# Optimization experiments

Measured on AMD Instinct MI355X. Metric: run time of the kernel, lower is better.

## Reference

```python
import jax, jax.numpy as jnp
import numpy as np

B, T, C, H = 4, 2048, 1024, 16
D = C // H  # head dim = 64


def setup_inputs() -> dict:
    key = jax.random.key(0)
    ks = jax.random.split(key, 5)
    s = 1.0 / np.sqrt(C)
    return {
        "x": jax.random.normal(ks[0], (B, T, C), dtype=jnp.float32),
        "Wq": jax.random.normal(ks[1], (C, C), dtype=jnp.float32) * s,
        "bq": jnp.zeros((C,), dtype=jnp.float32),
        "Wk": jax.random.normal(ks[2], (C, C), dtype=jnp.float32) * s,
        "bk": jnp.zeros((C,), dtype=jnp.float32),
        "Wv": jax.random.normal(ks[3], (C, C), dtype=jnp.float32) * s,
        "bv": jnp.zeros((C,), dtype=jnp.float32),
        "Wp": jax.random.normal(ks[4], (C, C), dtype=jnp.float32) * s,
        "bp": jnp.zeros((C,), dtype=jnp.float32),
    }


def reference(x, Wq, bq, Wk, bk, Wv, bv, Wp, bp):
    Bb, Tt, Cc = x.shape
    # QKV projections (torch Linear: y = x @ W.T + b)
    q = (x @ Wq.T + bq).reshape(Bb, Tt, H, D).transpose(0, 2, 1, 3)  # [B,H,T,D]
    k = (x @ Wk.T + bk).reshape(Bb, Tt, H, D).transpose(0, 2, 1, 3)
    v = (x @ Wv.T + bv).reshape(Bb, Tt, H, D).transpose(0, 2, 1, 3)
    att = jnp.einsum("bhqd,bhkd->bhqk", q, k) / jnp.sqrt(jnp.float32(D))
    causal = jnp.tril(jnp.ones((Tt, Tt), dtype=bool))
    att = jnp.where(causal[None, None], att, -jnp.inf)
    att = jax.nn.softmax(att, axis=-1)
    y = jnp.einsum("bhqk,bhkd->bhqd", att, v)  # [B,H,T,D]
    y = y.transpose(0, 2, 1, 3).reshape(Bb, Tt, Cc)
    return y @ Wp.T + bp
```

## Files before the change

kernel.cpp:

```cpp
#include <hip/hip_runtime.h>

typedef unsigned short u16;
typedef unsigned int u32;

typedef __attribute__((ext_vector_type(4))) float f32x4;
typedef __attribute__((ext_vector_type(8))) short bf16x8;


__device__ inline u16 f2b(float f) {
  union { float f; u32 u; } x; x.f = f;
  u32 u = x.u;
  u32 r = (u + 0x7fffu + ((u >> 16) & 1u)) >> 16;
  return (u16)r;
}

__device__ inline u32 cvtpk(float lo, float hi) {
  u32 r;
  asm("v_cvt_pk_bf16_f32 %0, %1, %2" : "=v"(r) : "v"(lo), "v"(hi));
  return r;
}

__device__ inline void gload_lds16(const void* g, void* l) {
  __builtin_amdgcn_global_load_lds(
      (const __attribute__((address_space(1))) u32*)g,
      (__attribute__((address_space(3))) u32*)l, 16, 0, 0);
}


__global__ __launch_bounds__(256) void cvt_all(const float* __restrict__ x,
                                               const float* __restrict__ w0,
                                               const float* __restrict__ w1,
                                               const float* __restrict__ w2,
                                               const float* __restrict__ w3,
                                               u16* __restrict__ xo,
                                               u16* __restrict__ wo) {
  int b = blockIdx.x;
  const float* s;
  u16* d;
  int i;
  if (b < 8192) {
    s = x; d = xo; i = b * 256 + threadIdx.x;
  } else {
    int m = (b - 8192) >> 10;
    s = (m == 0) ? w0 : (m == 1) ? w1 : (m == 2) ? w2 : w3;
    d = wo + (size_t)m * 1048576;
    i = ((b - 8192) & 1023) * 256 + threadIdx.x;
  }
  float4 v = ((const float4*)s)[i];
  ushort4 o;
  o.x = f2b(v.x); o.y = f2b(v.y); o.z = f2b(v.z); o.w = f2b(v.w);
  ((ushort4*)d)[i] = o;
}


__global__ __launch_bounds__(256) void gemm_qkv(const u16* __restrict__ A,
                                                const u16* __restrict__ W,
                                                const float* __restrict__ bq,
                                                const float* __restrict__ bk,
                                                const float* __restrict__ bv,
                                                u16* __restrict__ outQ,
                                                u16* __restrict__ outK,
                                                u16* __restrict__ outVt,
                                                float qscale) {
  __shared__ u16 sA[8192];
  __shared__ u16 sB[8192];

  const int K = 1024;
  const int t = threadIdx.x;
  const int lane = t & 63;
  const int w = t >> 6;
  const int wr = w >> 1, wc = w & 1;
  const int lr = lane & 15, lg = lane >> 4;

  int bid = blockIdx.y * 24 + blockIdx.x;
  int swz = (bid & 7) * 192 + (bid >> 3);
  const int mBase = (swz / 24) * 128;
  const int nBase = (swz % 24) * 128;
  const int mode = nBase >> 10;

  f32x4 zero = {0.f, 0.f, 0.f, 0.f};
  f32x4 acc[4][4];
#pragma unroll
  for (int i = 0; i < 4; ++i)
#pragma unroll
    for (int j = 0; j < 4; ++j) acc[i][j] = zero;

  const int rA = t >> 2;
  const int cA = (t & 3) * 8;

  for (int k0 = 0; k0 < K; k0 += 64) {
#pragma unroll
    for (int hh = 0; hh < 2; ++hh)
#pragma unroll
      for (int i = 0; i < 2; ++i) {
        gload_lds16(A + (size_t)(mBase + i * 64 + rA) * K + k0 + hh * 32 + cA,
                    &sA[hh * 4096 + i * 2048 + t * 8]);
        gload_lds16(W + (size_t)(nBase + i * 64 + rA) * K + k0 + hh * 32 + cA,
                    &sB[hh * 4096 + i * 2048 + t * 8]);
      }
    __syncthreads();

#pragma unroll
    for (int hh = 0; hh < 2; ++hh) {
      bf16x8 af[4], bf[4];
#pragma unroll
      for (int i = 0; i < 4; ++i)
        af[i] = *(const bf16x8*)&sA[hh * 4096 +
                                    (wr * 64 + i * 16 + lr) * 32 + lg * 8];
#pragma unroll
      for (int j = 0; j < 4; ++j)
        bf[j] = *(const bf16x8*)&sB[hh * 4096 +
                                    (wc * 64 + j * 16 + lr) * 32 + lg * 8];

#pragma unroll
      for (int i = 0; i < 4; ++i)
#pragma unroll
        for (int j = 0; j < 4; ++j)
          acc[i][j] = __builtin_amdgcn_mfma_f32_16x16x32_bf16(af[i], bf[j],
                                                              acc[i][j], 0, 0, 0);
    }
    __syncthreads();
  }

#pragma unroll
  for (int i = 0; i < 4; ++i) {
    int row = mBase + wr * 64 + i * 16 + lg * 4;
    int b = row >> 11, tp = row & 2047;
#pragma unroll
    for (int j = 0; j < 4; ++j) {
      int col = nBase + wc * 64 + j * 16 + lr;
      int ncol = col & 1023;
      int h = ncol >> 6, dd = ncol & 63;
      size_t bhOff = (size_t)(b * 16 + h) * 262144;
      if (mode == 2) {
        float bv_ = bv[ncol];
        ushort4 o;
        o.x = f2b(acc[i][j][0] + bv_);
        o.y = f2b(acc[i][j][1] + bv_);
        o.z = f2b(acc[i][j][2] + bv_);
        o.w = f2b(acc[i][j][3] + bv_);
        *(ushort4*)((char*)outVt + bhOff + (tp >> 6) * 8192 + dd * 128 +
                    ((((tp & 63) >> 3) << 4) ^ ((dd & 7) << 4)) +
                    (tp & 7) * 2) = o;
      } else if (mode == 0) {
        float bv_ = bq[ncol];
#pragma unroll
        for (int r = 0; r < 4; ++r)
          outQ[(((size_t)(b * 16 + h) * 2048) + tp + r) * 64 + dd] =
              f2b((acc[i][j][r] + bv_) * qscale);
      } else {
        float bv_ = bk[ncol];
#pragma unroll
        for (int r = 0; r < 4; ++r) {
          int tt = tp + r;
          *(u16*)((char*)outK + bhOff + (tt >> 6) * 8192 + (tt & 63) * 128 +
                  (((dd >> 3) << 4) ^ ((tt & 7) << 4)) + (dd & 7) * 2) =
              f2b(acc[i][j][r] + bv_);
        }
      }
    }
  }
}


__global__ __launch_bounds__(256) void gemm_proj(const u16* __restrict__ A,
                                                 const u16* __restrict__ W,
                                                 const float* __restrict__ bias,
                                                 float* __restrict__ outF) {
  __shared__ u16 sA[8192];
  __shared__ u16 sB[8192];

  const int K = 1024, N = 1024;
  const int t = threadIdx.x;
  const int lane = t & 63;
  const int w = t >> 6;
  const int wr = w >> 1, wc = w & 1;
  const int lr = lane & 15, lg = lane >> 4;

  int bid = blockIdx.y * 8 + blockIdx.x;
  int swz = (bid & 7) * 64 + (bid >> 3);
  const int mBase = (swz >> 3) * 128;
  const int nBase = (swz & 7) * 128;

  f32x4 zero = {0.f, 0.f, 0.f, 0.f};
  f32x4 acc[4][4];
#pragma unroll
  for (int i = 0; i < 4; ++i)
#pragma unroll
    for (int j = 0; j < 4; ++j) acc[i][j] = zero;

  const int rA = t >> 2;
  const int cA = (t & 3) * 8;

  for (int k0 = 0; k0 < K; k0 += 64) {
#pragma unroll
    for (int hh = 0; hh < 2; ++hh)
#pragma unroll
      for (int i = 0; i < 2; ++i) {
        gload_lds16(A + (size_t)(mBase + i * 64 + rA) * K + k0 + hh * 32 + cA,
                    &sA[hh * 4096 + i * 2048 + t * 8]);
        gload_lds16(W + (size_t)(nBase + i * 64 + rA) * K + k0 + hh * 32 + cA,
                    &sB[hh * 4096 + i * 2048 + t * 8]);
      }
    __syncthreads();

#pragma unroll
    for (int hh = 0; hh < 2; ++hh) {
      bf16x8 af[4], bf[4];
#pragma unroll
      for (int i = 0; i < 4; ++i)
        af[i] = *(const bf16x8*)&sA[hh * 4096 +
                                    (wr * 64 + i * 16 + lr) * 32 + lg * 8];
#pragma unroll
      for (int j = 0; j < 4; ++j)
        bf[j] = *(const bf16x8*)&sB[hh * 4096 +
                                    (wc * 64 + j * 16 + lr) * 32 + lg * 8];

#pragma unroll
      for (int i = 0; i < 4; ++i)
#pragma unroll
        for (int j = 0; j < 4; ++j)
          acc[i][j] = __builtin_amdgcn_mfma_f32_16x16x32_bf16(af[i], bf[j],
                                                              acc[i][j], 0, 0, 0);
    }
    __syncthreads();
  }

#pragma unroll
  for (int i = 0; i < 4; ++i) {
    int row = mBase + wr * 64 + i * 16 + lg * 4;
#pragma unroll
    for (int j = 0; j < 4; ++j) {
      int col = nBase + wc * 64 + j * 16 + lr;
      float bv = bias[col];
#pragma unroll
      for (int r = 0; r < 4; ++r)
        outF[(size_t)(row + r) * N + col] = acc[i][j][r] + bv;
    }
  }
}


__global__ __launch_bounds__(512) void attn_fwd(const u16* __restrict__ qg,
                                                const u16* __restrict__ kswz,
                                                const u16* __restrict__ vswz,
                                                u16* __restrict__ yg) {
  __shared__ u16 sK[2][64 * 64];
  __shared__ u16 sVt[2][64 * 64];

  const int t = threadIdx.x;
  const int lane = t & 63;
  const int w = t >> 6;
  const int lr = lane & 15, lg = lane >> 4;
  const int xk = (lr & 7) << 4;

  int bid0 = blockIdx.y * 8 + blockIdx.x;
  int swzb = (bid0 & 7) * 64 + (bid0 >> 3);
  const int bh = swzb >> 3;
  const int pair = swzb & 7;

  const char* kgb = (const char*)kswz + (size_t)bh * 262144;
  const char* vgb = (const char*)vswz + (size_t)bh * 262144;
  const u16* qb = qg + (size_t)bh * 131072;

  gload_lds16(kgb + t * 16, (char*)&sK[0][0] + t * 16);
  gload_lds16(vgb + t * 16, (char*)&sVt[0][0] + t * 16);

  f32x4 zero = {0.f, 0.f, 0.f, 0.f};
  const int b = bh >> 4, h = bh & 15;
  int tc = 0;

  for (int half = 0; half < 2; ++half) {
    const int qt = half ? pair : 15 - pair;
    const int nkt = 2 * qt + 2;
    const int wq0 = qt * 128 + w * 16;
    const int qrow = wq0 + lr;

    bf16x8 qf[2];
#pragma unroll
    for (int kk = 0; kk < 2; ++kk)
      qf[kk] = *(const bf16x8*)(qb + (size_t)qrow * 64 + kk * 32 + lg * 8);

    f32x4 accO[4];
#pragma unroll
    for (int n = 0; n < 4; ++n) accO[n] = zero;
    float lrun = 0.f;

    for (int kt = 0; kt < nkt; ++kt, ++tc) {
      const int cur = tc & 1;
      __syncthreads();

      int nextT = (kt + 1 < nkt) ? kt + 1 : (half == 0 ? 0 : -1);
      if (nextT >= 0) {
        gload_lds16(kgb + nextT * 8192 + t * 16,
                    (char*)&sK[cur ^ 1][0] + t * 16);
        gload_lds16(vgb + nextT * 8192 + t * 16,
                    (char*)&sVt[cur ^ 1][0] + t * 16);
      }

      if (kt * 64 > wq0 + 15) continue;

      const char* kb_ = (const char*)&sK[cur][0];
      const char* vb_ = (const char*)&sVt[cur][0];

      f32x4 s[4];
      __builtin_amdgcn_s_setprio(1);
#pragma unroll
      for (int n = 0; n < 4; ++n) {
        f32x4 a = zero;
#pragma unroll
        for (int kk = 0; kk < 2; ++kk) {
          bf16x8 kf = *(const bf16x8*)(kb_ + (n * 16 + lr) * 128 +
                                       ((kk * 64 + lg * 16) ^ xk));
          a = __builtin_amdgcn_mfma_f32_16x16x32_bf16(kf, qf[kk], a, 0, 0, 0);
        }
        s[n] = a;
      }
      __builtin_amdgcn_s_setprio(0);

      if (kt * 64 + 63 > wq0) {
#pragma unroll
        for (int n = 0; n < 4; ++n) {
          int key0 = kt * 64 + n * 16 + lg * 4;
#pragma unroll
          for (int r = 0; r < 4; ++r)
            s[n][r] = (key0 + r <= qrow) ? s[n][r] : -1e30f;
        }
      }

      u32 pk[4][2];
#pragma unroll
      for (int n = 0; n < 4; ++n) {
        float p0 = exp2f(s[n][0] - 12.f);
        float p1 = exp2f(s[n][1] - 12.f);
        float p2 = exp2f(s[n][2] - 12.f);
        float p3 = exp2f(s[n][3] - 12.f);
        lrun += (p0 + p1) + (p2 + p3);
        pk[n][0] = cvtpk(p0, p1);
        pk[n][1] = cvtpk(p2, p3);
      }

      const bool hi = (lg >> 1) & 1;
#pragma unroll
      for (int kk = 0; kk < 2; ++kk) {
        u32 g[4];
#pragma unroll
        for (int r = 0; r < 4; ++r) {
          const int rh = r >> 1, rl = r & 1;
          u32 give = ((lg & 1) ^ rh) ? pk[2 * kk + 1][rl] : pk[2 * kk][rl];
          int srcLane = ((lg & 1) * 2 + ((lg >> 1) ^ rh)) * 16 + lr;
          g[r] = (u32)__shfl((int)give, srcLane);
        }
        union { u32 u[4]; bf16x8 v; } pu;
        pu.u[0] = hi ? g[2] : g[0];
        pu.u[1] = hi ? g[3] : g[1];
        pu.u[2] = hi ? g[0] : g[2];
        pu.u[3] = hi ? g[1] : g[3];
        bf16x8 pf = pu.v;
        __builtin_amdgcn_s_setprio(1);
#pragma unroll
        for (int n = 0; n < 4; ++n) {
          bf16x8 vf = *(const bf16x8*)(vb_ + (n * 16 + lr) * 128 +
                                       ((kk * 64 + lg * 16) ^ xk));
          accO[n] = __builtin_amdgcn_mfma_f32_16x16x32_bf16(pf, vf, accO[n], 0, 0, 0);
        }
        __builtin_amdgcn_s_setprio(0);
      }
    }

    lrun += __shfl_xor(lrun, 16);
    lrun += __shfl_xor(lrun, 32);

#pragma unroll
    for (int r = 0; r < 4; ++r) {
      float linv = 1.f / __shfl(lrun, lg * 4 + r);
      int trow = qt * 128 + w * 16 + lg * 4 + r;
      size_t rowOff = ((size_t)b * 2048 + trow) * 1024 + h * 64;
#pragma unroll
      for (int n = 0; n < 4; ++n)
        yg[rowOff + n * 16 + lr] = f2b(accO[n][r] * linv);
    }
  }
}


extern "C" void kernel_launch(void* const* d_in, const int* in_sizes, int n_in,
                              void* d_out, int out_size, void* d_ws, size_t ws_size,
                              hipStream_t stream) {
  const float* x  = (const float*)d_in[0];
  const float* Wq = (const float*)d_in[1];
  const float* bq = (const float*)d_in[2];
  const float* Wk = (const float*)d_in[3];
  const float* bk = (const float*)d_in[4];
  const float* Wv = (const float*)d_in[5];
  const float* bv = (const float*)d_in[6];
  const float* Wp = (const float*)d_in[7];
  const float* bp = (const float*)d_in[8];
  float* out = (float*)d_out;

  char* ws = (char*)d_ws;
  u16* xb  = (u16*)(ws);
  u16* wqb = (u16*)(ws + (16u << 20));
  u16* wpb = (u16*)(ws + (22u << 20));
  u16* qb  = (u16*)(ws + (24u << 20));
  u16* kb  = (u16*)(ws + (40u << 20));
  u16* vtb = (u16*)(ws + (56u << 20));
  u16* yb  = (u16*)(ws + (72u << 20));

  const float SCL = 0.18033688011112042f;

  cvt_all<<<12288, 256, 0, stream>>>(x, Wq, Wk, Wv, Wp, xb, wqb);

  gemm_qkv<<<dim3(24, 64), 256, 0, stream>>>(xb, wqb, bq, bk, bv,
                                             qb, kb, vtb, SCL);

  attn_fwd<<<dim3(8, 64), 512, 0, stream>>>(qb, kb, vtb, yb);

  gemm_proj<<<dim3(8, 64), 256, 0, stream>>>(yb, wpb, bp, out);
}
```

Before: 188.1 us.

## Pre-swizzle QKV GEMM operands and double-buffer 256x256 tiles in LDS

The conversion kernel now writes x and the Q/K/V weights as bf16 in a tiled, XOR-swizzled layout. Each 256-row by 64-column K-slice becomes a contiguous 32 KB block, so the GEMM can stage it with linear global_load_lds copies. The QKV GEMM moves to 256x256 tiles with 512 threads and double-buffered LDS, prefetching the next K-slice while computing the current one, and raises MFMA issue priority with s_setprio. This is meant to cut global-load latency stalls and LDS bank conflicts, but it costs more LDS per block (128 KB), more accumulator registers, and fewer blocks, which may hurt occupancy and load balance.

```diff
diff --git a/kernel.cpp b/kernel.cpp
--- a/kernel.cpp
+++ b/kernel.cpp
@@ -32,29 +32,50 @@
                                                const float* __restrict__ w1,
                                                const float* __restrict__ w2,
                                                const float* __restrict__ w3,
-                                               u16* __restrict__ xo,
-                                               u16* __restrict__ wo) {
-  int b = blockIdx.x;
-  const float* s;
-  u16* d;
-  int i;
-  if (b < 8192) {
-    s = x; d = xo; i = b * 256 + threadIdx.x;
+                                               u16* __restrict__ xs,
+                                               u16* __restrict__ wsz,
+                                               u16* __restrict__ wp) {
+  int b = blockIdx.x, t = threadIdx.x;
+  const float* src;
+  char* dst;
+  if (b < 5632) {
+    int g = b * 256 + t;
+    int row;
+    if (b < 4096) {
+      row = g >> 7;
+      src = x + (size_t)row * 1024;
+      dst = (char*)xs;
+    } else {
+      g -= 1048576;
+      row = g >> 7;
+      src = (row < 1024) ? w0 + (size_t)row * 1024
+           : (row < 2048) ? w1 + (size_t)(row - 1024) * 1024
+                          : w2 + (size_t)(row - 2048) * 1024;
+      dst = (char*)wsz;
+    }
+    int c = g & 127;
+    int kt = c >> 3, cc = (c & 7) ^ (row & 7);
+    float4 lo = *(const float4*)(src + c * 8);
+    float4 hi = *(const float4*)(src + c * 8 + 4);
+    union { u16 s[8]; uint4 v; } o;
+    o.s[0] = f2b(lo.x); o.s[1] = f2b(lo.y); o.s[2] = f2b(lo.z); o.s[3] = f2b(lo.w);
+    o.s[4] = f2b(hi.x); o.s[5] = f2b(hi.y); o.s[6] = f2b(hi.z); o.s[7] = f2b(hi.w);
+    *(uint4*)(dst + (size_t)(row >> 8) * 524288 + kt * 32768 +
+              (row & 255) * 128 + cc * 16) = o.v;
   } else {
-    int m = (b - 8192) >> 10;
-    s = (m == 0) ? w0 : (m == 1) ? w1 : (m == 2) ? w2 : w3;
-    d = wo + (size_t)m * 1048576;
-    i = ((b - 8192) & 1023) * 256 + threadIdx.x;
-  }
-  float4 v = ((const float4*)s)[i];
-  ushort4 o;
-  o.x = f2b(v.x); o.y = f2b(v.y); o.z = f2b(v.z); o.w = f2b(v.w);
-  ((ushort4*)d)[i] = o;
-}
-
-
-__global__ __launch_bounds__(256) void gemm_qkv(const u16* __restrict__ A,
-                                                const u16* __restrict__ W,
+    int g = (b - 5632) * 256 + t;
+    float4 lo = *(const float4*)(w3 + (size_t)g * 8);
+    float4 hi = *(const float4*)(w3 + (size_t)g * 8 + 4);
+    union { u16 s[8]; uint4 v; } o;
+    o.s[0] = f2b(lo.x); o.s[1] = f2b(lo.y); o.s[2] = f2b(lo.z); o.s[3] = f2b(lo.w);
+    o.s[4] = f2b(hi.x); o.s[5] = f2b(hi.y); o.s[6] = f2b(hi.z); o.s[7] = f2b(hi.w);
+    *(uint4*)((char*)wp + (size_t)g * 16) = o.v;
+  }
+}
+
+
+__global__ __launch_bounds__(512) void gemm_qkv(const u16* __restrict__ Aswz,
+                                                const u16* __restrict__ Wswz,
                                                 const float* __restrict__ bq,
                                                 const float* __restrict__ bk,
                                                 const float* __restrict__ bv,
@@ -62,76 +83,105 @@
                                                 u16* __restrict__ outK,
                                                 u16* __restrict__ outVt,
                                                 float qscale) {
-  __shared__ u16 sA[8192];
-  __shared__ u16 sB[8192];
-
-  const int K = 1024;
+  __shared__ u16 sA[2][16384];
+  __shared__ u16 sB[2][16384];
+
   const int t = threadIdx.x;
   const int lane = t & 63;
   const int w = t >> 6;
-  const int wr = w >> 1, wc = w & 1;
+  const int wm = w >> 2, wn = w & 3;
   const int lr = lane & 15, lg = lane >> 4;
 
-  int bid = blockIdx.y * 24 + blockIdx.x;
-  int swz = (bid & 7) * 192 + (bid >> 3);
-  const int mBase = (swz / 24) * 128;
-  const int nBase = (swz % 24) * 128;
+  int bid = blockIdx.y * 12 + blockIdx.x;
+  int swz = (bid & 7) * 48 + (bid >> 3);
+  const int mBase = (swz / 12) * 256;
+  const int nBase = (swz % 12) * 256;
   const int mode = nBase >> 10;
 
-  f32x4 zero = {0.f, 0.f, 0.f, 0.f};
-  f32x4 acc[4][4];
-#pragma unroll
-  for (int i = 0; i < 4; ++i)
-#pragma unroll
-    for (int j = 0; j < 4; ++j) acc[i][j] = zero;
-
-  const int rA = t >> 2;
-  const int cA = (t & 3) * 8;
-
-  for (int k0 = 0; k0 < K; k0 += 64) {
-#pragma unroll
-    for (int hh = 0; hh < 2; ++hh)
-#pragma unroll
-      for (int i = 0; i < 2; ++i) {
-        gload_lds16(A + (size_t)(mBase + i * 64 + rA) * K + k0 + hh * 32 + cA,
-                    &sA[hh * 4096 + i * 2048 + t * 8]);
-        gload_lds16(W + (size_t)(nBase + i * 64 + rA) * K + k0 + hh * 32 + cA,
-                    &sB[hh * 4096 + i * 2048 + t * 8]);
-      }
-    __syncthreads();
-
-#pragma unroll
-    for (int hh = 0; hh < 2; ++hh) {
-      bf16x8 af[4], bf[4];
-#pragma unroll
-      for (int i = 0; i < 4; ++i)
-        af[i] = *(const bf16x8*)&sA[hh * 4096 +
-                                    (wr * 64 + i * 16 + lr) * 32 + lg * 8];
-#pragma unroll
-      for (int j = 0; j < 4; ++j)
-        bf[j] = *(const bf16x8*)&sB[hh * 4096 +
-                                    (wc * 64 + j * 16 + lr) * 32 + lg * 8];
-
-#pragma unroll
-      for (int i = 0; i < 4; ++i)
-#pragma unroll
-        for (int j = 0; j < 4; ++j)
-          acc[i][j] = __builtin_amdgcn_mfma_f32_16x16x32_bf16(af[i], bf[j],
-                                                              acc[i][j], 0, 0, 0);
-    }
-    __syncthreads();
-  }
-
-#pragma unroll
-  for (int i = 0; i < 4; ++i) {
-    int row = mBase + wr * 64 + i * 16 + lg * 4;
-    int b = row >> 11, tp = row & 2047;
+  const char* Ap = (const char*)Aswz + (size_t)(mBase >> 8) * 524288;
+  const char* Bp = (const char*)Wswz + (size_t)(nBase >> 8) * 524288;
+
+  f32x4 acc[8][4];
+#pragma unroll
+  for (int i = 0; i < 8; ++i)
+#pragma unroll
+    for (int j = 0; j < 4; ++j) acc[i][j] = (f32x4){0.f, 0.f, 0.f, 0.f};
+
+  auto stage8 = [&](int buf, int kt) {
+    const char* As = Ap + (size_t)kt * 32768;
+    const char* Bs = Bp + (size_t)kt * 32768;
+    char* Ad = (char*)&sA[buf][0];
+    char* Bd = (char*)&sB[buf][0];
+#pragma unroll
+    for (int l = 0; l < 4; ++l) {
+      int off = (l * 512 + t) * 16;
+      gload_lds16(As + off, Ad + off);
+      gload_lds16(Bs + off, Bd + off);
+    }
+  };
+
+  stage8(0, 0);
+  asm volatile("s_waitcnt vmcnt(0)" ::: "memory");
+  __builtin_amdgcn_s_barrier();
+
+  for (int kt = 0; kt < 16; ++kt) {
+    const int cur = kt & 1;
+    const char* Ab = (const char*)&sA[cur][0];
+    const char* Bb = (const char*)&sB[cur][0];
+
+#pragma unroll
+    for (int p = 0; p < 4; ++p) {
+      if (p == 0 && kt + 1 < 16) stage8(cur ^ 1, kt + 1);
+
+      const int qi = p >> 1, qj = p & 1;
+      bf16x8 af[4][2], bf[2][2];
+#pragma unroll
+      for (int ii = 0; ii < 4; ++ii) {
+        int row = wm * 128 + (qi * 4 + ii) * 16 + lr;
+#pragma unroll
+        for (int kk = 0; kk < 2; ++kk)
+          af[ii][kk] = *(const bf16x8*)(Ab + row * 128 +
+                                        ((kk * 64 + lg * 16) ^ ((row & 7) << 4)));
+      }
+#pragma unroll
+      for (int jj = 0; jj < 2; ++jj) {
+        int rn = wn * 64 + (qj * 2 + jj) * 16 + lr;
+#pragma unroll
+        for (int kk = 0; kk < 2; ++kk)
+          bf[jj][kk] = *(const bf16x8*)(Bb + rn * 128 +
+                                        ((kk * 64 + lg * 16) ^ ((rn & 7) << 4)));
+      }
+
+      __builtin_amdgcn_s_barrier();
+
+      __builtin_amdgcn_s_setprio(1);
+#pragma unroll
+      for (int ii = 0; ii < 4; ++ii)
+#pragma unroll
+        for (int jj = 0; jj < 2; ++jj)
+#pragma unroll
+          for (int kk = 0; kk < 2; ++kk)
+            acc[qi * 4 + ii][qj * 2 + jj] =
+                __builtin_amdgcn_mfma_f32_16x16x32_bf16(
+                    af[ii][kk], bf[jj][kk], acc[qi * 4 + ii][qj * 2 + jj],
+                    0, 0, 0);
+      __builtin_amdgcn_s_setprio(0);
+
+      if (p == 3) asm volatile("s_waitcnt vmcnt(0)" ::: "memory");
+      __builtin_amdgcn_s_barrier();
+    }
+  }
+
+#pragma unroll
+  for (int i = 0; i < 8; ++i) {
+    int row = mBase + wm * 128 + i * 16 + lg * 4;
+    int b_ = row >> 11, tp = row & 2047;
 #pragma unroll
     for (int j = 0; j < 4; ++j) {
-      int col = nBase + wc * 64 + j * 16 + lr;
+      int col = nBase + wn * 64 + j * 16 + lr;
       int ncol = col & 1023;
       int h = ncol >> 6, dd = ncol & 63;
-      size_t bhOff = (size_t)(b * 16 + h) * 262144;
+      size_t bhOff = (size_t)(b_ * 16 + h) * 262144;
       if (mode == 2) {
         float bv_ = bv[ncol];
         ushort4 o;
@@ -146,7 +196,7 @@
         float bv_ = bq[ncol];
 #pragma unroll
         for (int r = 0; r < 4; ++r)
-          outQ[(((size_t)(b * 16 + h) * 2048) + tp + r) * 64 + dd] =
+          outQ[(((size_t)(b_ * 16 + h) * 2048) + tp + r) * 64 + dd] =
               f2b((acc[i][j][r] + bv_) * qscale);
       } else {
         float bv_ = bk[ncol];
@@ -409,9 +459,9 @@
 
   const float SCL = 0.18033688011112042f;
 
-  cvt_all<<<12288, 256, 0, stream>>>(x, Wq, Wk, Wv, Wp, xb, wqb);
-
-  gemm_qkv<<<dim3(24, 64), 256, 0, stream>>>(xb, wqb, bq, bk, bv,
+  cvt_all<<<6144, 256, 0, stream>>>(x, Wq, Wk, Wv, Wp, xb, wqb, wpb);
+
+  gemm_qkv<<<dim3(12, 32), 512, 0, stream>>>(xb, wqb, bq, bk, bv,
                                              qb, kb, vtb, SCL);
 
   attn_fwd<<<dim3(8, 64), 512, 0, stream>>>(qb, kb, vtb, yb);
```

New measurement: 209.5 us. 11.4% more time.
